# Kernel tuning notes

Hardware: AMD Instinct MI355X
Metric: run time of the kernel (lower is better)

## Reference

```python
import jax, jax.numpy as jnp
import numpy as np

B, S, D_MODEL = 64, 2048, 512
NUM_UNITS = 512
WINDOW = 128  # attention_window_size


def setup_inputs() -> dict:
    key = jax.random.key(0)
    k1, k2, k3, k4, k5 = jax.random.split(key, 5)
    query = jax.random.normal(k1, (B, D_MODEL), dtype=jnp.float32)
    keys = jax.random.normal(k2, (B, S, D_MODEL), dtype=jnp.float32)
    key_lengths = jax.random.randint(k3, (B,), 0, 256, dtype=jnp.int32)
    Wq = jax.random.normal(k4, (NUM_UNITS, D_MODEL), dtype=jnp.float32) * 0.04
    wp = jax.random.normal(k5, (1, NUM_UNITS), dtype=jnp.float32) * 0.04
    return {"query": query, "keys": keys, "key_lengths": key_lengths, "Wq": Wq, "wp": wp}


def reference(query, keys, key_lengths, Wq, wp):
    # dot score: [B, S]
    score = jnp.einsum('bd,bsd->bs', query, keys)
    weight = jax.nn.softmax(score, axis=-1)

    # predictive local alignment
    L = key_lengths.astype(jnp.float32)[:, None]                      # [B, 1]
    activated = jnp.tanh(query @ Wq.T)                                # [B, num_units]
    sig = jax.nn.sigmoid(activated @ wp.T)                            # [B, 1]
    p = L * sig                                                       # [B, 1] predicted alignment point

    # window bounds via .int() truncation toward zero
    start = jnp.trunc(p - WINDOW).astype(jnp.int32)                   # [B, 1]
    end = jnp.trunc(p + WINDOW).astype(jnp.int32)                     # [B, 1]

    # gaussian factor (note: original uses L - p, a per-row scalar; 2*std = WINDOW)
    g = jnp.exp(-((L - p) ** 2) / WINDOW)                             # [B, 1]
    weight = weight * g                                               # [B, S]

    # per-row dynamic window gather + weighted sum, done as masked reduction
    pos = jnp.arange(S, dtype=jnp.int32)[None, :]                     # [1, S]
    mask = (pos >= start) & (pos < end)                               # [B, S]
    w = jnp.where(mask, weight, jnp.zeros((), dtype=weight.dtype))
    total_context = jnp.einsum('bs,bsd->bd', w, keys)                 # [B, d]
    return total_context, score
```

## Files before the change

### kernel.cpp

```cpp
#include <hip/hip_runtime.h>
#include <math.h>

#define BB 64
#define SS 2048
#define DD 512
#define NU 512
#define WIN 128
#define NSLICE 4
#define G_OFF   0
#define ST_OFF  64
#define EN_OFF  128
#define M_OFF   256
#define S_OFF   (256 + BB * 32)
#define PART_OFF 8192

__device__ __forceinline__ float wave_reduce_sum(float v) {
    #pragma unroll
    for (int off = 32; off > 0; off >>= 1)
        v += __shfl_down(v, off, 64);
    return v;
}

__device__ __forceinline__ float wave_reduce_max(float v) {
    #pragma unroll
    for (int off = 32; off > 0; off >>= 1)
        v = fmaxf(v, __shfl_down(v, off, 64));
    return v;
}

__device__ __forceinline__ float dot4(const float4 a, const float4 b) {
    return a.x * b.x + a.y * b.y + a.z * b.z + a.w * b.w;
}

__global__ __launch_bounds__(256, 4) void score_p_kernel(const float* __restrict__ query,
                                                         const float* __restrict__ keys,
                                                         const int* __restrict__ key_lengths,
                                                         const float* __restrict__ Wq,
                                                         const float* __restrict__ wp,
                                                         float* __restrict__ score,
                                                         float* __restrict__ ws) {
    const int t    = threadIdx.x;
    const int wave = t >> 6;
    const int lane = t & 63;
    const int g    = lane >> 4;
    const int w    = lane & 15;

    if (blockIdx.x < BB) {
        const int b = blockIdx.x;
        __shared__ float act[NU];
        __shared__ float wsum[4];

        const float4* qv = (const float4*)(query + b * DD);
        const float4 q0 = qv[w],       q1 = qv[16 + w],  q2 = qv[32 + w],  q3 = qv[48 + w];
        const float4 q4 = qv[64 + w],  q5 = qv[80 + w],  q6 = qv[96 + w],  q7 = qv[112 + w];

        #pragma unroll 2
        for (int pass = 0; pass < 32; ++pass) {
            const int u = pass * 16 + wave * 4 + g;
            const float4* rv = (const float4*)(Wq + (size_t)u * DD);
            const float4 k0 = rv[w],       k1 = rv[16 + w],  k2 = rv[32 + w],  k3 = rv[48 + w];
            const float4 k4 = rv[64 + w],  k5 = rv[80 + w],  k6 = rv[96 + w],  k7 = rv[112 + w];
            const float s0 = dot4(k0, q0), s1 = dot4(k1, q1), s2 = dot4(k2, q2), s3 = dot4(k3, q3);
            const float s4 = dot4(k4, q4), s5 = dot4(k5, q5), s6 = dot4(k6, q6), s7 = dot4(k7, q7);
            float acc = ((s0 + s1) + (s2 + s3)) + ((s4 + s5) + (s6 + s7));
            #pragma unroll
            for (int m = 1; m < 16; m <<= 1)
                acc += __shfl_xor(acc, m, 64);
            if (w == 0) act[u] = tanhf(acc);
        }
        __syncthreads();

        float sv = act[t] * wp[t] + act[t + 256] * wp[t + 256];
        sv = wave_reduce_sum(sv);
        if (lane == 0) wsum[wave] = sv;
        __syncthreads();

        if (t == 0) {
            const float s = wsum[0] + wsum[1] + wsum[2] + wsum[3];
            const float sig = 1.0f / (1.0f + expf(-s));
            const float L = (float)key_lengths[b];
            const float p = L * sig;
            const int start = (int)(p - (float)WIN);
            const int end   = (int)(p + (float)WIN);
            const float diff = L - p;
            const float gg = expf(-(diff * diff) / (float)WIN);
            ws[G_OFF + b] = gg;
            ((int*)ws)[ST_OFF + b] = start;
            ((int*)ws)[EN_OFF + b] = end;
        }
    } else {
        const int bid   = blockIdx.x - BB;
        const int b     = bid >> 5;
        const int chunk = bid & 31;
        const int r0    = chunk * 64 + wave * 16;
        __shared__ float sc_l[64];

        const float4* qv = (const float4*)(query + b * DD);
        const float4 q0 = qv[w],       q1 = qv[16 + w],  q2 = qv[32 + w],  q3 = qv[48 + w];
        const float4 q4 = qv[64 + w],  q5 = qv[80 + w],  q6 = qv[96 + w],  q7 = qv[112 + w];

        const float4* kb = (const float4*)(keys + (size_t)b * SS * DD);

        const float4* rv = kb + (size_t)(r0 + g) * (DD / 4);
        float4 k0 = rv[w],       k1 = rv[16 + w],  k2 = rv[32 + w],  k3 = rv[48 + w];
        float4 k4 = rv[64 + w],  k5 = rv[80 + w],  k6 = rv[96 + w],  k7 = rv[112 + w];

        #pragma unroll
        for (int p = 0; p < 4; ++p) {
            float4 n0, n1, n2, n3, n4, n5, n6, n7;
            if (p < 3) {
                const float4* nv = kb + (size_t)(r0 + (p + 1) * 4 + g) * (DD / 4);
                n0 = nv[w];       n1 = nv[16 + w];  n2 = nv[32 + w];  n3 = nv[48 + w];
                n4 = nv[64 + w];  n5 = nv[80 + w];  n6 = nv[96 + w];  n7 = nv[112 + w];
            }
            const float s0 = dot4(k0, q0), s1 = dot4(k1, q1), s2 = dot4(k2, q2), s3 = dot4(k3, q3);
            const float s4 = dot4(k4, q4), s5 = dot4(k5, q5), s6 = dot4(k6, q6), s7 = dot4(k7, q7);
            float acc = ((s0 + s1) + (s2 + s3)) + ((s4 + s5) + (s6 + s7));
            #pragma unroll
            for (int m = 1; m < 16; m <<= 1)
                acc += __shfl_xor(acc, m, 64);
            if (w == 0) {
                score[b * SS + r0 + p * 4 + g] = acc;
                sc_l[wave * 16 + p * 4 + g] = acc;
            }
            if (p < 3) {
                k0 = n0; k1 = n1; k2 = n2; k3 = n3;
                k4 = n4; k5 = n5; k6 = n6; k7 = n7;
            }
        }
        __syncthreads();

        if (t < 64) {
            const float v = sc_l[t];
            float m = wave_reduce_max(v);
            const float mloc = __shfl(m, 0, 64);
            const float ssum = wave_reduce_sum(expf(v - mloc));
            if (t == 0) {
                ws[M_OFF + b * 32 + chunk] = mloc;
                ws[S_OFF + b * 32 + chunk] = ssum;
            }
        }
    }
}

__global__ __launch_bounds__(512) void ctxA_kernel(const float* __restrict__ keys,
                                                   const float* __restrict__ score,
                                                   const float* __restrict__ ws,
                                                   float* __restrict__ part) {
    const int b     = blockIdx.x;
    const int slice = blockIdx.y;
    const int t     = threadIdx.x;
    const int wave  = t >> 6;
    const int lane  = t & 63;

    __shared__ float w_lds[72];
    __shared__ float stat_l[2];
    __shared__ float4 part_l[3][128];

    if (wave == 0) {
        const float mi = (lane < 32) ? ws[M_OFF + b * 32 + lane] : -INFINITY;
        float m = wave_reduce_max(mi);
        const float mx0 = __shfl(m, 0, 64);
        const float si = (lane < 32) ? ws[S_OFF + b * 32 + lane] * expf(mi - mx0) : 0.f;
        float s = wave_reduce_sum(si);
        if (lane == 0) { stat_l[0] = mx0; stat_l[1] = 1.0f / s; }
    }
    __syncthreads();
    const float mx  = stat_l[0];
    const float inv = stat_l[1];

    const float gg   = ws[G_OFF + b];
    const int start  = ((const int*)ws)[ST_OFF + b];
    const int end    = ((const int*)ws)[EN_OFF + b];
    const int s_lo   = max(start, 0);
    const int s_hi   = min(end, SS);
    const int width  = s_hi - s_lo;
    const int sliceN = (width + NSLICE - 1) / NSLICE;
    const int i_lo   = slice * sliceN;
    const int i_hi   = min(i_lo + sliceN, width);
    const int n      = i_hi - i_lo;

    const float* srow = score + b * SS;
    for (int i = t; i < n; i += 512)
        w_lds[i] = expf(srow[s_lo + i_lo + i] - mx) * inv * gg;
    __syncthreads();

    const int myrow = t >> 7;
    const int c4    = t & 127;
    const float4* kb = (const float4*)(keys + ((size_t)b * SS + s_lo + i_lo) * DD);

    float4 acc = make_float4(0.f, 0.f, 0.f, 0.f);
    for (int i = myrow; i < n; i += 4) {
        const float4 k = kb[(size_t)i * (DD / 4) + c4];
        const float wg = w_lds[i];
        acc.x += wg * k.x; acc.y += wg * k.y; acc.z += wg * k.z; acc.w += wg * k.w;
    }

    if (myrow) part_l[myrow - 1][c4] = acc;
    __syncthreads();
    if (myrow == 0) {
        #pragma unroll
        for (int r = 0; r < 3; ++r) {
            const float4 o = part_l[r][c4];
            acc.x += o.x; acc.y += o.y; acc.z += o.z; acc.w += o.w;
        }
        ((float4*)part)[((size_t)b * NSLICE + slice) * 128 + c4] = acc;
    }
}

__global__ __launch_bounds__(512) void ctxB_kernel(const float* __restrict__ part,
                                                   float* __restrict__ ctx) {
    const int b = blockIdx.x;
    const int d = threadIdx.x;
    float s = 0.f;
    #pragma unroll
    for (int sl = 0; sl < NSLICE; ++sl)
        s += part[((size_t)b * NSLICE + sl) * DD + d];
    ctx[b * DD + d] = s;
}

extern "C" void kernel_launch(void* const* d_in, const int* in_sizes, int n_in,
                              void* d_out, int out_size, void* d_ws, size_t ws_size,
                              hipStream_t stream) {
    const float* query       = (const float*)d_in[0];
    const float* keys        = (const float*)d_in[1];
    const int*   key_lengths = (const int*)d_in[2];
    const float* Wq          = (const float*)d_in[3];
    const float* wp          = (const float*)d_in[4];

    float* ctx   = (float*)d_out;
    float* score = (float*)d_out + BB * DD;
    float* ws    = (float*)d_ws;
    float* part  = (float*)d_ws + PART_OFF;

    hipLaunchKernelGGL(score_p_kernel, dim3(BB + BB * 32), dim3(256), 0, stream,
                       query, keys, key_lengths, Wq, wp, score, ws);
    hipLaunchKernelGGL(ctxA_kernel, dim3(BB, NSLICE), dim3(512), 0, stream,
                       keys, score, ws, part);
    hipLaunchKernelGGL(ctxB_kernel, dim3(BB), dim3(512), 0, stream,
                       part, ctx);
}
```

Measured before the change: 62.63 us.

## Split context reduction over feature columns to drop the partial-sum kernel

The context kernel now splits work across blocks by 128-column chunks of the feature dimension rather than by slices of the window. Each block reduces over the whole window, so it writes its final output directly and the second reduction kernel, along with its workspace round-trip, is removed. The cost is scalar loads instead of float4 loads and a longer serial loop per block. The weight vector is also recomputed once per column chunk.

```diff
diff --git a/kernel.cpp b/kernel.cpp
--- a/kernel.cpp
+++ b/kernel.cpp
@@ -6,13 +6,11 @@
 #define DD 512
 #define NU 512
 #define WIN 128
-#define NSLICE 4
 #define G_OFF   0
 #define ST_OFF  64
 #define EN_OFF  128
 #define M_OFF   256
 #define S_OFF   (256 + BB * 32)
-#define PART_OFF 8192
 
 __device__ __forceinline__ float wave_reduce_sum(float v) {
     #pragma unroll
@@ -143,19 +141,19 @@
     }
 }
 
-__global__ __launch_bounds__(512) void ctxA_kernel(const float* __restrict__ keys,
-                                                   const float* __restrict__ score,
-                                                   const float* __restrict__ ws,
-                                                   float* __restrict__ part) {
-    const int b     = blockIdx.x;
-    const int slice = blockIdx.y;
-    const int t     = threadIdx.x;
-    const int wave  = t >> 6;
-    const int lane  = t & 63;
-
-    __shared__ float w_lds[72];
+__global__ __launch_bounds__(512) void ctx_kernel(const float* __restrict__ keys,
+                                                  const float* __restrict__ score,
+                                                  const float* __restrict__ ws,
+                                                  float* __restrict__ ctx) {
+    const int b      = blockIdx.x;
+    const int dchunk = blockIdx.y;
+    const int t      = threadIdx.x;
+    const int wave   = t >> 6;
+    const int lane   = t & 63;
+
+    __shared__ float w_lds[260];
     __shared__ float stat_l[2];
-    __shared__ float4 part_l[3][128];
+    __shared__ float part_l[3][128];
 
     if (wave == 0) {
         const float mi = (lane < 32) ? ws[M_OFF + b * 32 + lane] : -INFINITY;
@@ -175,48 +173,27 @@
     const int s_lo   = max(start, 0);
     const int s_hi   = min(end, SS);
     const int width  = s_hi - s_lo;
-    const int sliceN = (width + NSLICE - 1) / NSLICE;
-    const int i_lo   = slice * sliceN;
-    const int i_hi   = min(i_lo + sliceN, width);
-    const int n      = i_hi - i_lo;
 
     const float* srow = score + b * SS;
-    for (int i = t; i < n; i += 512)
-        w_lds[i] = expf(srow[s_lo + i_lo + i] - mx) * inv * gg;
+    for (int i = t; i < width; i += 512)
+        w_lds[i] = expf(srow[s_lo + i] - mx) * inv * gg;
     __syncthreads();
 
-    const int myrow = t >> 7;
-    const int c4    = t & 127;
-    const float4* kb = (const float4*)(keys + ((size_t)b * SS + s_lo + i_lo) * DD);
-
-    float4 acc = make_float4(0.f, 0.f, 0.f, 0.f);
-    for (int i = myrow; i < n; i += 4) {
-        const float4 k = kb[(size_t)i * (DD / 4) + c4];
-        const float wg = w_lds[i];
-        acc.x += wg * k.x; acc.y += wg * k.y; acc.z += wg * k.z; acc.w += wg * k.w;
+    const int r  = t >> 7;
+    const int c  = t & 127;
+    const float* kb = keys + ((size_t)b * SS + s_lo) * DD + dchunk * 128;
+
+    float acc = 0.f;
+    for (int i = r; i < width; i += 4)
+        acc += w_lds[i] * kb[(size_t)i * DD + c];
+
+    if (r) part_l[r - 1][c] = acc;
+    __syncthreads();
+    if (r == 0) {
+        #pragma unroll
+        for (int j = 0; j < 3; ++j) acc += part_l[j][c];
+        ctx[b * DD + dchunk * 128 + c] = acc;
     }
-
-    if (myrow) part_l[myrow - 1][c4] = acc;
-    __syncthreads();
-    if (myrow == 0) {
-        #pragma unroll
-        for (int r = 0; r < 3; ++r) {
-            const float4 o = part_l[r][c4];
-            acc.x += o.x; acc.y += o.y; acc.z += o.z; acc.w += o.w;
-        }
-        ((float4*)part)[((size_t)b * NSLICE + slice) * 128 + c4] = acc;
-    }
-}
-
-__global__ __launch_bounds__(512) void ctxB_kernel(const float* __restrict__ part,
-                                                   float* __restrict__ ctx) {
-    const int b = blockIdx.x;
-    const int d = threadIdx.x;
-    float s = 0.f;
-    #pragma unroll
-    for (int sl = 0; sl < NSLICE; ++sl)
-        s += part[((size_t)b * NSLICE + sl) * DD + d];
-    ctx[b * DD + d] = s;
 }
 
 extern "C" void kernel_launch(void* const* d_in, const int* in_sizes, int n_in,
@@ -231,12 +208,9 @@
     float* ctx   = (float*)d_out;
     float* score = (float*)d_out + BB * DD;
     float* ws    = (float*)d_ws;
-    float* part  = (float*)d_ws + PART_OFF;
 
     hipLaunchKernelGGL(score_p_kernel, dim3(BB + BB * 32), dim3(256), 0, stream,
                        query, keys, key_lengths, Wq, wp, score, ws);
-    hipLaunchKernelGGL(ctxA_kernel, dim3(BB, NSLICE), dim3(512), 0, stream,
-                       keys, score, ws, part);
-    hipLaunchKernelGGL(ctxB_kernel, dim3(BB), dim3(512), 0, stream,
-                       part, ctx);
-}
+    hipLaunchKernelGGL(ctx_kernel, dim3(BB, 4), dim3(512), 0, stream,
+                       keys, score, ws, ctx);
+}
```

Result: slower. 72.06 us (+15.1%).
